# Optimization experiments

Hardware: AMD Instinct MI355X
Metric: run time of the kernel (lower is better)

## Reference

```python
import jax, jax.numpy as jnp
import numpy as np

N, E, F_IN, H, C, L = 100000, 1600000, 128, 64, 16, 3
NEG_SLOPE_ATT = 0.2   # GATConv attention leaky_relu
NEG_SLOPE_ACT = 0.01  # F.leaky_relu default


def setup_inputs() -> dict:
    key = jax.random.key(0)
    ks = jax.random.split(key, 12)
    x = jax.random.normal(ks[0], (N, F_IN), dtype=jnp.float32)
    edge_index = jax.random.randint(ks[1], (2, E), 0, N, dtype=jnp.int64)
    edge_weight = jax.random.uniform(ks[2], (E,), dtype=jnp.float32)
    s = 0.05
    W_in = jax.random.normal(ks[3], (F_IN, H), dtype=jnp.float32) * s
    b_in = jnp.zeros((H,), dtype=jnp.float32)
    Wc = jax.random.normal(ks[4], (L, H, H), dtype=jnp.float32) * s
    a_src = jax.random.normal(ks[5], (L, H), dtype=jnp.float32) * s
    a_dst = jax.random.normal(ks[6], (L, H), dtype=jnp.float32) * s
    bc = jnp.zeros((L, H), dtype=jnp.float32)
    W_out = jax.random.normal(ks[7], (H, C), dtype=jnp.float32) * s
    b_out = jnp.zeros((C,), dtype=jnp.float32)
    return {"x": x, "edge_index": edge_index, "edge_weight": edge_weight,
            "W_in": W_in, "b_in": b_in, "Wc": Wc, "a_src": a_src,
            "a_dst": a_dst, "bc": bc, "W_out": W_out, "b_out": b_out}


def _gat_layer(h, src, dst, W, asrc, adst, b):
    # linear transform (no bias on lin in PyG GATConv)
    h = h @ W                                   # [N, H]
    # per-node attention contributions
    alpha_s = h @ asrc                          # [N]
    alpha_d = h @ adst                          # [N]
    e = jax.nn.leaky_relu(alpha_s[src] + alpha_d[dst], NEG_SLOPE_ATT)  # [E']
    # segment softmax over destination nodes
    m = jax.ops.segment_max(e, dst, num_segments=N)
    ex = jnp.exp(e - m[dst])
    denom = jax.ops.segment_sum(ex, dst, num_segments=N)
    w = ex / (denom[dst] + 1e-16)
    # weighted scatter-add aggregation
    out = jax.ops.segment_sum(h[src] * w[:, None], dst, num_segments=N)
    return out + b


def reference(x, edge_index, edge_weight, W_in, b_in, Wc, a_src, a_dst, bc, W_out, b_out):
    # add self-loops (PyG GATConv default)
    loops = jnp.arange(N, dtype=edge_index.dtype)
    src = jnp.concatenate([edge_index[0], loops])
    dst = jnp.concatenate([edge_index[1], loops])

    h = jax.nn.leaky_relu(x @ W_in + b_in, NEG_SLOPE_ACT)
    for l in range(L):
        h = jax.nn.leaky_relu(_gat_layer(h, src, dst, Wc[l], a_src[l], a_dst[l], bc[l]), NEG_SLOPE_ACT)
    logits = h @ W_out + b_out
    return jax.nn.log_softmax(logits, axis=-1)
```

## Files before the change

kernel.cpp:

```cpp
#include <hip/hip_runtime.h>

#define N_NODES 100000
#define E_EDGES 1600000
#define F_IN    128
#define H_DIM   64
#define C_OUT   16
#define L_LAYERS 3
#define NTOT    (E_EDGES + N_NODES)
#define MAXD    64

#define BKN2    512
#define NB2     ((N_NODES + BKN2 - 1) / BKN2)
#define BCAP    9216
#define CH      8192
#define PB      ((E_EDGES + CH - 1) / CH)

typedef __attribute__((ext_vector_type(8))) short short8;
typedef __attribute__((ext_vector_type(4))) float f32x4;

__device__ inline unsigned short f2bf(float f) {
    unsigned u = __float_as_uint(f);
    return (unsigned short)((u + 0x7FFFu + ((u >> 16) & 1u)) >> 16);
}
__device__ inline float bf_lo(unsigned p) { return __uint_as_float(p << 16); }
__device__ inline float bf_hi(unsigned p) { return __uint_as_float(p & 0xFFFF0000u); }
__device__ inline unsigned cvt_pk_bf16(float lo, float hi) {
    unsigned r;
    asm("v_cvt_pk_bf16_f32 %0, %1, %2" : "=v"(r) : "v"(lo), "v"(hi));
    return r;
}

__global__ void detect64_kernel(const unsigned int* __restrict__ e, int* flag) {
    __shared__ int s_any;
    if (threadIdx.x == 0) s_any = 0;
    __syncthreads();
    int any = 0;
    for (int i = threadIdx.x; i < 2048; i += 256)
        if (e[2 * i + 1] != 0u) any = 1;
    if (any) atomicOr(&s_any, 1);
    __syncthreads();
    if (threadIdx.x == 0) *flag = s_any ? 0 : 1;
}

__global__ __launch_bounds__(256) void bucket_scatter2(
        const void* __restrict__ eidx, const int* __restrict__ flag,
        int* __restrict__ bcur, unsigned int* __restrict__ packed) {
    __shared__ int cnt[NB2], basel[NB2], curl[NB2], gbase[NB2];
    __shared__ int sd[256];
    __shared__ unsigned int stage[CH];
    __shared__ unsigned char bkt[CH];
    int t = threadIdx.x;
    int b0 = blockIdx.x * CH;
    int ne = min(CH, E_EDGES - b0);
    for (int i = t; i < NB2; i += 256) cnt[i] = 0;
    __syncthreads();

    int f64 = *flag;
    int es[CH / 256], ed[CH / 256];
    #pragma unroll
    for (int j = 0; j < CH / 256; ++j) {
        int idx = b0 + j * 256 + t;
        if (idx < E_EDGES) {
            if (f64) {
                es[j] = (int)((const long long*)eidx)[idx];
                ed[j] = (int)((const long long*)eidx)[E_EDGES + idx];
            } else {
                es[j] = ((const int*)eidx)[idx];
                ed[j] = ((const int*)eidx)[E_EDGES + idx];
            }
            atomicAdd(&cnt[ed[j] >> 9], 1);
        } else { es[j] = -1; }
    }
    __syncthreads();
    int v = (t < NB2) ? cnt[t] : 0;
    sd[t] = v;
    __syncthreads();
    for (int off = 1; off < 256; off <<= 1) {
        int u = (t >= off) ? sd[t - off] : 0;
        __syncthreads();
        sd[t] += u;
        __syncthreads();
    }
    if (t < NB2) {
        basel[t] = sd[t] - v;
        curl[t] = 0;
        gbase[t] = atomicAdd(&bcur[t], v);
    }
    __syncthreads();
    #pragma unroll
    for (int j = 0; j < CH / 256; ++j) {
        if (es[j] >= 0) {
            int b = ed[j] >> 9;
            int r = atomicAdd(&curl[b], 1);
            int pos = basel[b] + r;
            stage[pos] = ((unsigned)(ed[j] & (BKN2 - 1)) << 17) | (unsigned)es[j];
            bkt[pos] = (unsigned char)b;
        }
    }
    __syncthreads();
    for (int i = t; i < ne; i += 256) {
        int b = bkt[i];
        packed[(size_t)b * BCAP + gbase[b] + (i - basel[b])] = stage[i];
    }
}

__global__ __launch_bounds__(256) void bucket_scan2(
        const int* __restrict__ bcur, int* __restrict__ ebase) {
    __shared__ int sd[256];
    int t = threadIdx.x;
    int v = (t < NB2) ? bcur[t] : 0;
    sd[t] = v;
    __syncthreads();
    for (int off = 1; off < 256; off <<= 1) {
        int u = (t >= off) ? sd[t - off] : 0;
        __syncthreads();
        sd[t] += u;
        __syncthreads();
    }
    if (t < NB2) ebase[t] = sd[t] - v;
}

__global__ __launch_bounds__(256) void csr_build2(
        const unsigned int* __restrict__ packed, const int* __restrict__ bcur,
        const int* __restrict__ ebase,
        int* __restrict__ row_ptr, int* __restrict__ csr_src) {
    __shared__ int cnt[BKN2], scn[BKN2], cur[BKN2];
    int b = blockIdx.x, t = threadIdx.x;
    int nbase = b * BKN2;
    int nn = min(BKN2, N_NODES - nbase);
    int ec = bcur[b];
    size_t pbase = (size_t)b * BCAP;
    int cbase = ebase[b] + nbase;
    cnt[t] = (t < nn) ? 1 : 0;
    cnt[t + 256] = (t + 256 < nn) ? 1 : 0;
    __syncthreads();
    for (int i = t; i < ec; i += 256)
        atomicAdd(&cnt[packed[pbase + i] >> 17], 1);
    __syncthreads();
    scn[t] = cnt[t];
    scn[t + 256] = cnt[t + 256];
    __syncthreads();
    for (int off = 1; off < BKN2; off <<= 1) {
        int u0 = (t >= off) ? scn[t - off] : 0;
        int u1 = (t + 256 >= off) ? scn[t + 256 - off] : 0;
        __syncthreads();
        scn[t] += u0;
        scn[t + 256] += u1;
        __syncthreads();
    }
    #pragma unroll
    for (int q = 0; q < 2; ++q) {
        int idx = t + q * 256;
        if (idx < nn) {
            int offi = scn[idx] - cnt[idx];
            row_ptr[nbase + idx] = cbase + offi;
            csr_src[cbase + offi] = nbase + idx;
            cur[idx] = offi + 1;
        }
    }
    if (b == NB2 - 1 && t == 0) row_ptr[N_NODES] = cbase + ec + nn;
    __syncthreads();
    for (int i = t; i < ec; i += 256) {
        unsigned p = packed[pbase + i];
        int dl = p >> 17, s = (int)(p & 0x1FFFFu);
        int pos = atomicAdd(&cur[dl], 1);
        csr_src[cbase + pos] = s;
    }
}

#define GBR 64
#define KC  64
#define SAP (KC + 4)

__global__ __launch_bounds__(256) void gemm_in_kernel(
        const float* __restrict__ A, const float* __restrict__ W,
        const float* __restrict__ bias, unsigned* __restrict__ C) {
    __shared__ __align__(16) float sW[KC * 64];
    __shared__ __align__(16) float sA[GBR][SAP];
    int t = threadIdx.x;
    int r0 = blockIdx.x * GBR;
    int wave = t >> 6, lane = t & 63;
    int tr = wave * 4 + (lane >> 4);
    int c0 = (lane & 15) * 4;

    float acc[4][4];
    #pragma unroll
    for (int i = 0; i < 4; ++i)
        #pragma unroll
        for (int j = 0; j < 4; ++j) acc[i][j] = 0.f;

    for (int kc = 0; kc < F_IN; kc += KC) {
        if (kc) __syncthreads();
        {
            const float4* W4 = (const float4*)(W + kc * 64);
            float4* sW4 = (float4*)sW;
            for (int i = t; i < KC * 16; i += 256) sW4[i] = W4[i];
        }
        for (int it = 0; it < (GBR * KC / 4) / 256; ++it) {
            int idx = it * 256 + t;
            int r = idx >> 4;
            int c4 = idx & 15;
            int gr = r0 + r;
            float4 v = make_float4(0.f, 0.f, 0.f, 0.f);
            if (gr < N_NODES) v = *(const float4*)&A[(size_t)gr * F_IN + kc + c4 * 4];
            *(float4*)&sA[r][c4 * 4] = v;
        }
        __syncthreads();
        #pragma unroll 2
        for (int kk = 0; kk < KC; kk += 4) {
            float4 w0 = *(const float4*)&sW[(kk + 0) * 64 + c0];
            float4 w1 = *(const float4*)&sW[(kk + 1) * 64 + c0];
            float4 w2 = *(const float4*)&sW[(kk + 2) * 64 + c0];
            float4 w3 = *(const float4*)&sW[(kk + 3) * 64 + c0];
            #pragma unroll
            for (int i = 0; i < 4; ++i) {
                float4 a = *(const float4*)&sA[tr + 16 * i][kk];
                acc[i][0] += a.x * w0.x + a.y * w1.x + a.z * w2.x + a.w * w3.x;
                acc[i][1] += a.x * w0.y + a.y * w1.y + a.z * w2.y + a.w * w3.y;
                acc[i][2] += a.x * w0.z + a.y * w1.z + a.z * w2.z + a.w * w3.z;
                acc[i][3] += a.x * w0.w + a.y * w1.w + a.z * w2.w + a.w * w3.w;
            }
        }
    }

    float bs[4];
    #pragma unroll
    for (int j = 0; j < 4; ++j) bs[j] = bias[c0 + j];
    #pragma unroll
    for (int i = 0; i < 4; ++i) {
        int grow = r0 + tr + 16 * i;
        if (grow >= N_NODES) continue;
        float v0 = acc[i][0] + bs[0]; v0 = v0 > 0.f ? v0 : 0.01f * v0;
        float v1 = acc[i][1] + bs[1]; v1 = v1 > 0.f ? v1 : 0.01f * v1;
        float v2 = acc[i][2] + bs[2]; v2 = v2 > 0.f ? v2 : 0.01f * v2;
        float v3 = acc[i][3] + bs[3]; v3 = v3 > 0.f ? v3 : 0.01f * v3;
        *(uint2*)&C[(size_t)grow * 32 + (c0 >> 1)] =
            make_uint2(cvt_pk_bf16(v0, v1), cvt_pk_bf16(v2, v3));
    }
}

__global__ __launch_bounds__(256) void gemm_mfma_kernel(
        const unsigned* __restrict__ A32, const float* __restrict__ W,
        const float* __restrict__ asrc, const float* __restrict__ adst,
        unsigned* __restrict__ C, float* __restrict__ as_, float* __restrict__ ad_) {
    __shared__ __align__(16) unsigned short sWT[64][72];
    __shared__ float sAv[64], sDv[64];
    __shared__ __align__(16) float sTile[4][16 * 64];
    int t = threadIdx.x;
    for (int i = t; i < 64 * 64; i += 256) {
        int k = i >> 6, j = i & 63;
        sWT[j][k] = f2bf(W[i]);
    }
    if (t < 64) { sAv[t] = asrc[t]; sDv[t] = adst[t]; }
    __syncthreads();

    int wave = t >> 6, lane = t & 63;
    int r0 = blockIdx.x * 64 + wave * 16;
    int cj = lane & 15, kq = lane >> 4;

    int ra = r0 + cj;
    if (ra >= N_NODES) ra = N_NODES - 1;
    const short8* arow = (const short8*)&A32[(size_t)ra * 32];
    short8 a0 = arow[kq];
    short8 a1 = arow[4 + kq];

    f32x4 zero = {0.f, 0.f, 0.f, 0.f};
    f32x4 acc[4] = {zero, zero, zero, zero};
    #pragma unroll
    for (int ct = 0; ct < 4; ++ct) {
        short8 b0 = *(const short8*)&sWT[16 * ct + cj][kq * 8];
        short8 b1 = *(const short8*)&sWT[16 * ct + cj][32 + kq * 8];
        acc[ct] = __builtin_amdgcn_mfma_f32_16x16x32_bf16(a0, b0, acc[ct], 0, 0, 0);
        acc[ct] = __builtin_amdgcn_mfma_f32_16x16x32_bf16(a1, b1, acc[ct], 0, 0, 0);
    }

    float av[4], dv[4];
    #pragma unroll
    for (int ct = 0; ct < 4; ++ct) { av[ct] = sAv[ct * 16 + cj]; dv[ct] = sDv[ct * 16 + cj]; }
    #pragma unroll
    for (int r = 0; r < 4; ++r) {
        float ds = acc[0][r] * av[0] + acc[1][r] * av[1] + acc[2][r] * av[2] + acc[3][r] * av[3];
        float dd = acc[0][r] * dv[0] + acc[1][r] * dv[1] + acc[2][r] * dv[2] + acc[3][r] * dv[3];
        #pragma unroll
        for (int off = 1; off < 16; off <<= 1) {
            ds += __shfl_xor(ds, off);
            dd += __shfl_xor(dd, off);
        }
        int grow = r0 + kq * 4 + r;
        if (cj == 0 && grow < N_NODES) { as_[grow] = ds; ad_[grow] = dd; }
    }

    float* tl = sTile[wave];
    #pragma unroll
    for (int ct = 0; ct < 4; ++ct)
        #pragma unroll
        for (int r = 0; r < 4; ++r)
            tl[(kq * 4 + r) * 64 + ct * 16 + cj] = acc[ct][r];
    unsigned ur[8];
    #pragma unroll
    for (int i = 0; i < 8; ++i) {
        float2 fp = *(const float2*)&tl[(lane * 8 + i) * 2];
        ur[i] = cvt_pk_bf16(fp.x, fp.y);
    }
    int grow = r0 + (lane >> 2);
    if (grow < N_NODES) {
        uint4* dst = (uint4*)&C[(size_t)grow * 32 + (lane & 3) * 8];
        dst[0] = make_uint4(ur[0], ur[1], ur[2], ur[3]);
        dst[1] = make_uint4(ur[4], ur[5], ur[6], ur[7]);
    }
}

__global__ __launch_bounds__(256) void agg_kernel(
        const int* __restrict__ row_ptr, const int* __restrict__ csr_src,
        const float* __restrict__ as_, const float* __restrict__ ad_,
        const unsigned* __restrict__ hw32, const float* __restrict__ bc,
        unsigned* __restrict__ hout32) {
    __shared__ float exbuf[4][MAXD];
    __shared__ int   sbuf[4][MAXD];
    int wave = threadIdx.x >> 6, lane = threadIdx.x & 63;
    int node = blockIdx.x * 4 + wave;
    if (node >= N_NODES) return;
    int rs = row_ptr[node], re = row_ptr[node + 1];
    int deg = re - rs;
    float aD = ad_[node];
    float psum = 0.f;
    for (int i = lane; i < deg; i += 64) {
        int s = csr_src[rs + i];
        float v = as_[s] + aD;
        v = v > 0.f ? v : 0.2f * v;
        float p = __expf(v);
        if (deg <= MAXD) { exbuf[wave][i] = p; sbuf[wave][i] = s; }
        psum += p;
    }
    #pragma unroll
    for (int off = 32; off >= 1; off >>= 1) psum += __shfl_xor(psum, off);
    float inv = 1.f / (psum + 1e-16f);

    int half = lane >> 5, fl = lane & 31;
    float acc0 = 0.f, acc1 = 0.f;
    if (deg <= MAXD) {
        int i = half;
        for (; i + 6 < deg; i += 8) {
            unsigned o0 = ((unsigned)sbuf[wave][i]     << 5) | fl;
            unsigned o1 = ((unsigned)sbuf[wave][i + 2] << 5) | fl;
            unsigned o2 = ((unsigned)sbuf[wave][i + 4] << 5) | fl;
            unsigned o3 = ((unsigned)sbuf[wave][i + 6] << 5) | fl;
            float w0 = exbuf[wave][i],     w1 = exbuf[wave][i + 2];
            float w2 = exbuf[wave][i + 4], w3 = exbuf[wave][i + 6];
            unsigned p0 = hw32[o0];
            unsigned p1 = hw32[o1];
            unsigned p2 = hw32[o2];
            unsigned p3 = hw32[o3];
            acc0 += w0 * bf_lo(p0) + w1 * bf_lo(p1) + w2 * bf_lo(p2) + w3 * bf_lo(p3);
            acc1 += w0 * bf_hi(p0) + w1 * bf_hi(p1) + w2 * bf_hi(p2) + w3 * bf_hi(p3);
        }
        for (; i < deg; i += 2) {
            float w = exbuf[wave][i];
            unsigned p = hw32[((unsigned)sbuf[wave][i] << 5) | fl];
            acc0 += w * bf_lo(p);
            acc1 += w * bf_hi(p);
        }
    } else {
        for (int i = half; i < deg; i += 2) {
            int s = csr_src[rs + i];
            float v = as_[s] + aD;
            v = v > 0.f ? v : 0.2f * v;
            float w = __expf(v);
            unsigned p = hw32[((unsigned)s << 5) | fl];
            acc0 += w * bf_lo(p);
            acc1 += w * bf_hi(p);
        }
    }
    acc0 += __shfl_xor(acc0, 32);
    acc1 += __shfl_xor(acc1, 32);
    if (half == 0) {
        float v0 = acc0 * inv + bc[2 * fl];
        float v1 = acc1 * inv + bc[2 * fl + 1];
        v0 = v0 > 0.f ? v0 : 0.01f * v0;
        v1 = v1 > 0.f ? v1 : 0.01f * v1;
        hout32[((unsigned)node << 5) | fl] = cvt_pk_bf16(v0, v1);
    }
}

__global__ __launch_bounds__(256) void out_logsoftmax_kernel(
        const unsigned* __restrict__ h32, const float* __restrict__ W,
        const float* __restrict__ b, float* __restrict__ out) {
    __shared__ float sW[H_DIM * C_OUT];
    __shared__ float sh[16][H_DIM];
    __shared__ float sb[C_OUT];
    int t = threadIdx.x;
    for (int i = t; i < H_DIM * C_OUT; i += 256) sW[i] = W[i];
    if (t < C_OUT) sb[t] = b[t];
    int row0 = blockIdx.x * 16;
    #pragma unroll
    for (int it = 0; it < 2; ++it) {
        int idx = it * 256 + t;
        int r = idx >> 5, c2 = idx & 31;
        unsigned u = h32[((unsigned)(row0 + r) << 5) | c2];
        sh[r][c2 * 2] = bf_lo(u);
        sh[r][c2 * 2 + 1] = bf_hi(u);
    }
    __syncthreads();
    int r = t >> 4, c = t & 15;
    float acc = sb[c];
    #pragma unroll
    for (int k = 0; k < H_DIM; ++k) acc += sh[r][k] * sW[k * C_OUT + c];
    float m = acc;
    #pragma unroll
    for (int off = 8; off >= 1; off >>= 1) m = fmaxf(m, __shfl_xor(m, off, 16));
    float e = __expf(acc - m);
    float ssum = e;
    #pragma unroll
    for (int off = 8; off >= 1; off >>= 1) ssum += __shfl_xor(ssum, off, 16);
    out[(row0 + r) * C_OUT + c] = acc - m - __logf(ssum);
}

extern "C" void kernel_launch(void* const* d_in, const int* in_sizes, int n_in,
                              void* d_out, int out_size, void* d_ws, size_t ws_size,
                              hipStream_t stream) {
    const float* x     = (const float*)d_in[0];
    const void*  eidx  = d_in[1];
    const float* W_in  = (const float*)d_in[3];
    const float* b_in  = (const float*)d_in[4];
    const float* Wc    = (const float*)d_in[5];
    const float* a_src = (const float*)d_in[6];
    const float* a_dst = (const float*)d_in[7];
    const float* bc    = (const float*)d_in[8];
    const float* W_out = (const float*)d_in[9];
    const float* b_out = (const float*)d_in[10];
    float* out = (float*)d_out;

    unsigned* h     = (unsigned*)d_ws;
    unsigned* hw    = h + (size_t)N_NODES * 32;
    float* as_      = (float*)(hw + (size_t)N_NODES * 32);
    float* ad_      = as_ + N_NODES;
    int*   row_ptr  = (int*)(ad_ + N_NODES);
    int*   csr_src  = row_ptr + N_NODES + 1;
    unsigned int* packed = (unsigned int*)(csr_src + NTOT);
    int*   bcur     = (int*)(packed + (size_t)NB2 * BCAP);
    int*   ebase    = bcur + NB2;
    int*   flag     = ebase + NB2;

    detect64_kernel<<<1, 256, 0, stream>>>((const unsigned int*)eidx, flag);
    hipMemsetAsync(bcur, 0, NB2 * sizeof(int), stream);
    bucket_scatter2<<<PB, 256, 0, stream>>>(eidx, flag, bcur, packed);
    bucket_scan2<<<1, 256, 0, stream>>>(bcur, ebase);
    csr_build2<<<NB2, 256, 0, stream>>>(packed, bcur, ebase, row_ptr, csr_src);

    gemm_in_kernel<<<(N_NODES + GBR - 1) / GBR, 256, 0, stream>>>(x, W_in, b_in, h);

    unsigned* hin = h;
    unsigned* hx  = hw;
    int mblocks = (N_NODES + 63) / 64;
    for (int l = 0; l < L_LAYERS; ++l) {
        gemm_mfma_kernel<<<mblocks, 256, 0, stream>>>(
            hin, Wc + l * H_DIM * H_DIM,
            a_src + l * H_DIM, a_dst + l * H_DIM, hx, as_, ad_);
        agg_kernel<<<(N_NODES + 3) / 4, 256, 0, stream>>>(
            row_ptr, csr_src, as_, ad_, hx, bc + l * H_DIM, hin);
    }

    out_logsoftmax_kernel<<<N_NODES / 16, 256, 0, stream>>>(hin, W_out, b_out, out);
}
```

Measured before the change: 303.8 us.

## Use MFMA input GEMM, fuse int64 detection and bucket scan, widen aggregation loads

Replaces the fp32 FMA input GEMM with a bf16 MFMA kernel that converts x and a transposed W_in to bf16 in shared memory. The separate int64-detection and bucket-scan kernels are removed: each scatter block samples its own edge chunk, and each CSR build block reduces the preceding bucket counts itself. The aggregation kernel now has four edge groups per wave, each loading 4 bf16 features with uint2 loads. Shared tiles are padded to a stride of 65 to avoid bank conflicts. These changes cut launches and FMA work, at the cost of bf16 rounding of x and W_in and a heavier shuffle reduction.

```diff
diff --git a/kernel.cpp b/kernel.cpp
--- a/kernel.cpp
+++ b/kernel.cpp
@@ -30,32 +30,30 @@
     return r;
 }
 
-__global__ void detect64_kernel(const unsigned int* __restrict__ e, int* flag) {
-    __shared__ int s_any;
-    if (threadIdx.x == 0) s_any = 0;
-    __syncthreads();
-    int any = 0;
-    for (int i = threadIdx.x; i < 2048; i += 256)
-        if (e[2 * i + 1] != 0u) any = 1;
-    if (any) atomicOr(&s_any, 1);
-    __syncthreads();
-    if (threadIdx.x == 0) *flag = s_any ? 0 : 1;
-}
-
 __global__ __launch_bounds__(256) void bucket_scatter2(
-        const void* __restrict__ eidx, const int* __restrict__ flag,
+        const void* __restrict__ eidx,
         int* __restrict__ bcur, unsigned int* __restrict__ packed) {
     __shared__ int cnt[NB2], basel[NB2], curl[NB2], gbase[NB2];
     __shared__ int sd[256];
+    __shared__ int sflag;
     __shared__ unsigned int stage[CH];
     __shared__ unsigned char bkt[CH];
     int t = threadIdx.x;
     int b0 = blockIdx.x * CH;
     int ne = min(CH, E_EDGES - b0);
+    if (t == 0) sflag = 0;
     for (int i = t; i < NB2; i += 256) cnt[i] = 0;
     __syncthreads();
-
-    int f64 = *flag;
+    {
+        int nsamp = min(ne, 1024);
+        int any = 0;
+        for (int j = t; j < nsamp; j += 256)
+            if (((const unsigned*)eidx)[2 * (size_t)(b0 + j) + 1] != 0u) any = 1;
+        if (any) atomicOr(&sflag, 1);
+    }
+    __syncthreads();
+    int f64 = sflag ? 0 : 1;
+
     int es[CH / 256], ed[CH / 256];
     #pragma unroll
     for (int j = 0; j < CH / 256; ++j) {
@@ -104,33 +102,25 @@
     }
 }
 
-__global__ __launch_bounds__(256) void bucket_scan2(
-        const int* __restrict__ bcur, int* __restrict__ ebase) {
-    __shared__ int sd[256];
-    int t = threadIdx.x;
-    int v = (t < NB2) ? bcur[t] : 0;
-    sd[t] = v;
-    __syncthreads();
-    for (int off = 1; off < 256; off <<= 1) {
-        int u = (t >= off) ? sd[t - off] : 0;
-        __syncthreads();
-        sd[t] += u;
-        __syncthreads();
-    }
-    if (t < NB2) ebase[t] = sd[t] - v;
-}
-
 __global__ __launch_bounds__(256) void csr_build2(
         const unsigned int* __restrict__ packed, const int* __restrict__ bcur,
-        const int* __restrict__ ebase,
         int* __restrict__ row_ptr, int* __restrict__ csr_src) {
     __shared__ int cnt[BKN2], scn[BKN2], cur[BKN2];
     int b = blockIdx.x, t = threadIdx.x;
+    scn[t] = (t < b) ? bcur[t] : 0;
+    __syncthreads();
+    for (int off = 128; off >= 1; off >>= 1) {
+        if (t < off) scn[t] += scn[t + off];
+        __syncthreads();
+    }
+    int ebase_b = scn[0];
+    __syncthreads();
+
     int nbase = b * BKN2;
     int nn = min(BKN2, N_NODES - nbase);
     int ec = bcur[b];
     size_t pbase = (size_t)b * BCAP;
-    int cbase = ebase[b] + nbase;
+    int cbase = ebase_b + nbase;
     cnt[t] = (t < nn) ? 1 : 0;
     cnt[t + 256] = (t + 256 < nn) ? 1 : 0;
     __syncthreads();
@@ -168,74 +158,78 @@
     }
 }
 
-#define GBR 64
-#define KC  64
-#define SAP (KC + 4)
-
-__global__ __launch_bounds__(256) void gemm_in_kernel(
-        const float* __restrict__ A, const float* __restrict__ W,
+#define SAW 136
+
+__global__ __launch_bounds__(256) void gemm_in_mfma(
+        const float* __restrict__ X, const float* __restrict__ W,
         const float* __restrict__ bias, unsigned* __restrict__ C) {
-    __shared__ __align__(16) float sW[KC * 64];
-    __shared__ __align__(16) float sA[GBR][SAP];
+    __shared__ __align__(16) unsigned short sA[64][SAW];
+    __shared__ __align__(16) unsigned short sWT[64][SAW];
+    __shared__ float sB[64];
     int t = threadIdx.x;
-    int r0 = blockIdx.x * GBR;
+    int r0 = blockIdx.x * 64;
+    #pragma unroll
+    for (int it = 0; it < 8; ++it) {
+        int idx = it * 256 + t;
+        int r = idx >> 5, c4 = (idx & 31) * 4;
+        int gr = r0 + r;
+        float4 v = make_float4(0.f, 0.f, 0.f, 0.f);
+        if (gr < N_NODES) v = *(const float4*)&X[(size_t)gr * F_IN + c4];
+        unsigned* dst = (unsigned*)&sA[r][c4];
+        dst[0] = cvt_pk_bf16(v.x, v.y);
+        dst[1] = cvt_pk_bf16(v.z, v.w);
+    }
+    #pragma unroll
+    for (int it = 0; it < 8; ++it) {
+        int idx = it * 256 + t;
+        int k = idx >> 4, j4 = (idx & 15) * 4;
+        float4 v = *(const float4*)&W[k * 64 + j4];
+        sWT[j4 + 0][k] = f2bf(v.x);
+        sWT[j4 + 1][k] = f2bf(v.y);
+        sWT[j4 + 2][k] = f2bf(v.z);
+        sWT[j4 + 3][k] = f2bf(v.w);
+    }
+    if (t < 64) sB[t] = bias[t];
+    __syncthreads();
+
     int wave = t >> 6, lane = t & 63;
-    int tr = wave * 4 + (lane >> 4);
-    int c0 = (lane & 15) * 4;
-
-    float acc[4][4];
-    #pragma unroll
-    for (int i = 0; i < 4; ++i)
+    int cj = lane & 15, kq = lane >> 4;
+    int lrow = wave * 16 + cj;
+    f32x4 zero = {0.f, 0.f, 0.f, 0.f};
+    f32x4 acc[4] = {zero, zero, zero, zero};
+    #pragma unroll
+    for (int q = 0; q < 4; ++q) {
+        short8 a = *(const short8*)&sA[lrow][q * 32 + kq * 8];
         #pragma unroll
-        for (int j = 0; j < 4; ++j) acc[i][j] = 0.f;
-
-    for (int kc = 0; kc < F_IN; kc += KC) {
-        if (kc) __syncthreads();
-        {
-            const float4* W4 = (const float4*)(W + kc * 64);
-            float4* sW4 = (float4*)sW;
-            for (int i = t; i < KC * 16; i += 256) sW4[i] = W4[i];
-        }
-        for (int it = 0; it < (GBR * KC / 4) / 256; ++it) {
-            int idx = it * 256 + t;
-            int r = idx >> 4;
-            int c4 = idx & 15;
-            int gr = r0 + r;
-            float4 v = make_float4(0.f, 0.f, 0.f, 0.f);
-            if (gr < N_NODES) v = *(const float4*)&A[(size_t)gr * F_IN + kc + c4 * 4];
-            *(float4*)&sA[r][c4 * 4] = v;
-        }
-        __syncthreads();
-        #pragma unroll 2
-        for (int kk = 0; kk < KC; kk += 4) {
-            float4 w0 = *(const float4*)&sW[(kk + 0) * 64 + c0];
-            float4 w1 = *(const float4*)&sW[(kk + 1) * 64 + c0];
-            float4 w2 = *(const float4*)&sW[(kk + 2) * 64 + c0];
-            float4 w3 = *(const float4*)&sW[(kk + 3) * 64 + c0];
-            #pragma unroll
-            for (int i = 0; i < 4; ++i) {
-                float4 a = *(const float4*)&sA[tr + 16 * i][kk];
-                acc[i][0] += a.x * w0.x + a.y * w1.x + a.z * w2.x + a.w * w3.x;
-                acc[i][1] += a.x * w0.y + a.y * w1.y + a.z * w2.y + a.w * w3.y;
-                acc[i][2] += a.x * w0.z + a.y * w1.z + a.z * w2.z + a.w * w3.z;
-                acc[i][3] += a.x * w0.w + a.y * w1.w + a.z * w2.w + a.w * w3.w;
-            }
-        }
-    }
-
-    float bs[4];
-    #pragma unroll
-    for (int j = 0; j < 4; ++j) bs[j] = bias[c0 + j];
-    #pragma unroll
-    for (int i = 0; i < 4; ++i) {
-        int grow = r0 + tr + 16 * i;
-        if (grow >= N_NODES) continue;
-        float v0 = acc[i][0] + bs[0]; v0 = v0 > 0.f ? v0 : 0.01f * v0;
-        float v1 = acc[i][1] + bs[1]; v1 = v1 > 0.f ? v1 : 0.01f * v1;
-        float v2 = acc[i][2] + bs[2]; v2 = v2 > 0.f ? v2 : 0.01f * v2;
-        float v3 = acc[i][3] + bs[3]; v3 = v3 > 0.f ? v3 : 0.01f * v3;
-        *(uint2*)&C[(size_t)grow * 32 + (c0 >> 1)] =
-            make_uint2(cvt_pk_bf16(v0, v1), cvt_pk_bf16(v2, v3));
+        for (int ct = 0; ct < 4; ++ct) {
+            short8 bfr = *(const short8*)&sWT[ct * 16 + cj][q * 32 + kq * 8];
+            acc[ct] = __builtin_amdgcn_mfma_f32_16x16x32_bf16(a, bfr, acc[ct], 0, 0, 0);
+        }
+    }
+    __syncthreads();
+    float* tl = (float*)&sA[0][0] + wave * (16 * 65);
+    #pragma unroll
+    for (int ct = 0; ct < 4; ++ct) {
+        float bsv = sB[ct * 16 + cj];
+        #pragma unroll
+        for (int r = 0; r < 4; ++r) {
+            float v = acc[ct][r] + bsv;
+            v = v > 0.f ? v : 0.01f * v;
+            tl[(kq * 4 + r) * 65 + ct * 16 + cj] = v;
+        }
+    }
+    unsigned ur[8];
+    int trow = lane >> 2, tcb = lane & 3;
+    #pragma unroll
+    for (int i = 0; i < 8; ++i) {
+        float2 fp = *(const float2*)&tl[trow * 65 + tcb * 16 + i * 2];
+        ur[i] = cvt_pk_bf16(fp.x, fp.y);
+    }
+    int grow = r0 + wave * 16 + trow;
+    if (grow < N_NODES) {
+        uint4* dst = (uint4*)&C[(size_t)grow * 32 + tcb * 8];
+        dst[0] = make_uint4(ur[0], ur[1], ur[2], ur[3]);
+        dst[1] = make_uint4(ur[4], ur[5], ur[6], ur[7]);
     }
 }
 
@@ -245,7 +239,7 @@
         unsigned* __restrict__ C, float* __restrict__ as_, float* __restrict__ ad_) {
     __shared__ __align__(16) unsigned short sWT[64][72];
     __shared__ float sAv[64], sDv[64];
-    __shared__ __align__(16) float sTile[4][16 * 64];
+    __shared__ __align__(16) float sTile[4][16 * 65];
     int t = threadIdx.x;
     for (int i = t; i < 64 * 64; i += 256) {
         int k = i >> 6, j = i & 63;
@@ -295,16 +289,17 @@
     for (int ct = 0; ct < 4; ++ct)
         #pragma unroll
         for (int r = 0; r < 4; ++r)
-            tl[(kq * 4 + r) * 64 + ct * 16 + cj] = acc[ct][r];
+            tl[(kq * 4 + r) * 65 + ct * 16 + cj] = acc[ct][r];
     unsigned ur[8];
+    int trow = lane >> 2, tcb = lane & 3;
     #pragma unroll
     for (int i = 0; i < 8; ++i) {
-        float2 fp = *(const float2*)&tl[(lane * 8 + i) * 2];
+        float2 fp = *(const float2*)&tl[trow * 65 + tcb * 16 + i * 2];
         ur[i] = cvt_pk_bf16(fp.x, fp.y);
     }
-    int grow = r0 + (lane >> 2);
+    int grow = r0 + trow;
     if (grow < N_NODES) {
-        uint4* dst = (uint4*)&C[(size_t)grow * 32 + (lane & 3) * 8];
+        uint4* dst = (uint4*)&C[(size_t)grow * 32 + tcb * 8];
         dst[0] = make_uint4(ur[0], ur[1], ur[2], ur[3]);
         dst[1] = make_uint4(ur[4], ur[5], ur[6], ur[7]);
     }
@@ -336,49 +331,54 @@
     for (int off = 32; off >= 1; off >>= 1) psum += __shfl_xor(psum, off);
     float inv = 1.f / (psum + 1e-16f);
 
-    int half = lane >> 5, fl = lane & 31;
-    float acc0 = 0.f, acc1 = 0.f;
+    int g = lane >> 4, fl16 = lane & 15;
+    float a0 = 0.f, a1 = 0.f, a2 = 0.f, a3 = 0.f;
     if (deg <= MAXD) {
-        int i = half;
-        for (; i + 6 < deg; i += 8) {
-            unsigned o0 = ((unsigned)sbuf[wave][i]     << 5) | fl;
-            unsigned o1 = ((unsigned)sbuf[wave][i + 2] << 5) | fl;
-            unsigned o2 = ((unsigned)sbuf[wave][i + 4] << 5) | fl;
-            unsigned o3 = ((unsigned)sbuf[wave][i + 6] << 5) | fl;
-            float w0 = exbuf[wave][i],     w1 = exbuf[wave][i + 2];
-            float w2 = exbuf[wave][i + 4], w3 = exbuf[wave][i + 6];
-            unsigned p0 = hw32[o0];
-            unsigned p1 = hw32[o1];
-            unsigned p2 = hw32[o2];
-            unsigned p3 = hw32[o3];
-            acc0 += w0 * bf_lo(p0) + w1 * bf_lo(p1) + w2 * bf_lo(p2) + w3 * bf_lo(p3);
-            acc1 += w0 * bf_hi(p0) + w1 * bf_hi(p1) + w2 * bf_hi(p2) + w3 * bf_hi(p3);
-        }
-        for (; i < deg; i += 2) {
+        int i = g;
+        for (; i + 4 < deg; i += 8) {
+            float w0 = exbuf[wave][i], w1 = exbuf[wave][i + 4];
+            int s0 = sbuf[wave][i], s1 = sbuf[wave][i + 4];
+            uint2 p0 = *(const uint2*)&hw32[((unsigned)s0 << 5) | (fl16 * 2)];
+            uint2 p1 = *(const uint2*)&hw32[((unsigned)s1 << 5) | (fl16 * 2)];
+            a0 += w0 * bf_lo(p0.x) + w1 * bf_lo(p1.x);
+            a1 += w0 * bf_hi(p0.x) + w1 * bf_hi(p1.x);
+            a2 += w0 * bf_lo(p0.y) + w1 * bf_lo(p1.y);
+            a3 += w0 * bf_hi(p0.y) + w1 * bf_hi(p1.y);
+        }
+        for (; i < deg; i += 4) {
             float w = exbuf[wave][i];
-            unsigned p = hw32[((unsigned)sbuf[wave][i] << 5) | fl];
-            acc0 += w * bf_lo(p);
-            acc1 += w * bf_hi(p);
+            int s = sbuf[wave][i];
+            uint2 p = *(const uint2*)&hw32[((unsigned)s << 5) | (fl16 * 2)];
+            a0 += w * bf_lo(p.x);
+            a1 += w * bf_hi(p.x);
+            a2 += w * bf_lo(p.y);
+            a3 += w * bf_hi(p.y);
         }
     } else {
-        for (int i = half; i < deg; i += 2) {
+        for (int i = g; i < deg; i += 4) {
             int s = csr_src[rs + i];
             float v = as_[s] + aD;
             v = v > 0.f ? v : 0.2f * v;
             float w = __expf(v);
-            unsigned p = hw32[((unsigned)s << 5) | fl];
-            acc0 += w * bf_lo(p);
-            acc1 += w * bf_hi(p);
-        }
-    }
-    acc0 += __shfl_xor(acc0, 32);
-    acc1 += __shfl_xor(acc1, 32);
-    if (half == 0) {
-        float v0 = acc0 * inv + bc[2 * fl];
-        float v1 = acc1 * inv + bc[2 * fl + 1];
-        v0 = v0 > 0.f ? v0 : 0.01f * v0;
-        v1 = v1 > 0.f ? v1 : 0.01f * v1;
-        hout32[((unsigned)node << 5) | fl] = cvt_pk_bf16(v0, v1);
+            uint2 p = *(const uint2*)&hw32[((unsigned)s << 5) | (fl16 * 2)];
+            a0 += w * bf_lo(p.x);
+            a1 += w * bf_hi(p.x);
+            a2 += w * bf_lo(p.y);
+            a3 += w * bf_hi(p.y);
+        }
+    }
+    a0 += __shfl_xor(a0, 16); a0 += __shfl_xor(a0, 32);
+    a1 += __shfl_xor(a1, 16); a1 += __shfl_xor(a1, 32);
+    a2 += __shfl_xor(a2, 16); a2 += __shfl_xor(a2, 32);
+    a3 += __shfl_xor(a3, 16); a3 += __shfl_xor(a3, 32);
+    if (g == 0) {
+        float4 bv = *(const float4*)&bc[fl16 * 4];
+        float v0 = a0 * inv + bv.x; v0 = v0 > 0.f ? v0 : 0.01f * v0;
+        float v1 = a1 * inv + bv.y; v1 = v1 > 0.f ? v1 : 0.01f * v1;
+        float v2 = a2 * inv + bv.z; v2 = v2 > 0.f ? v2 : 0.01f * v2;
+        float v3 = a3 * inv + bv.w; v3 = v3 > 0.f ? v3 : 0.01f * v3;
+        *(uint2*)&hout32[((unsigned)node << 5) | (fl16 * 2)] =
+            make_uint2(cvt_pk_bf16(v0, v1), cvt_pk_bf16(v2, v3));
     }
 }
 
@@ -438,16 +438,12 @@
     int*   csr_src  = row_ptr + N_NODES + 1;
     unsigned int* packed = (unsigned int*)(csr_src + NTOT);
     int*   bcur     = (int*)(packed + (size_t)NB2 * BCAP);
-    int*   ebase    = bcur + NB2;
-    int*   flag     = ebase + NB2;
-
-    detect64_kernel<<<1, 256, 0, stream>>>((const unsigned int*)eidx, flag);
+
     hipMemsetAsync(bcur, 0, NB2 * sizeof(int), stream);
-    bucket_scatter2<<<PB, 256, 0, stream>>>(eidx, flag, bcur, packed);
-    bucket_scan2<<<1, 256, 0, stream>>>(bcur, ebase);
-    csr_build2<<<NB2, 256, 0, stream>>>(packed, bcur, ebase, row_ptr, csr_src);
-
-    gemm_in_kernel<<<(N_NODES + GBR - 1) / GBR, 256, 0, stream>>>(x, W_in, b_in, h);
+    bucket_scatter2<<<PB, 256, 0, stream>>>(eidx, bcur, packed);
+    csr_build2<<<NB2, 256, 0, stream>>>(packed, bcur, row_ptr, csr_src);
+
+    gemm_in_mfma<<<(N_NODES + 63) / 64, 256, 0, stream>>>(x, W_in, b_in, h);
 
     unsigned* hin = h;
     unsigned* hx  = hw;
```

New measurement: 297.5 us. -2.1%, faster.
